# Optimization experiments

Hardware: AMD Instinct MI355X
Metric: run time of the kernel (lower is better)

## Reference

```python
import jax, jax.numpy as jnp
import numpy as np

N, F, H = 4096, 512, 64
TEMP = 1.0
EPS = 1e-6


def _lin_init(k, fi, fo):
    s = 1.0 / np.sqrt(fi)
    return jax.random.uniform(k, (fi, fo), jnp.float32, -s, s)


def setup_inputs() -> dict:
    key = jax.random.key(0)
    ks = jax.random.split(key, 8)
    adj = jax.random.uniform(ks[0], (N, N), jnp.float32)
    adj = 0.5 * (adj + adj.T)  # symmetric dense adjacency
    x = jax.random.normal(ks[1], (N, F), jnp.float32)
    return {
        'adj': adj,
        'x': x,
        'Wg': _lin_init(ks[2], F, H), 'bg': jnp.zeros((H,), jnp.float32),
        'Wa1': _lin_init(ks[3], H, H), 'ba1': jnp.zeros((H,), jnp.float32),
        'Wa2': _lin_init(ks[4], H, F), 'ba2': jnp.zeros((F,), jnp.float32),
        'Wx1': _lin_init(ks[5], H, H), 'bx1': jnp.zeros((H,), jnp.float32),
        'Wx2': _lin_init(ks[6], H, F), 'bx2': jnp.zeros((F,), jnp.float32),
    }


def _relaxed_bernoulli_st(probs, noise_logistic, temp):
    # pyro RelaxedBernoulliStraightThrough.rsample(): gumbel-sigmoid + hard round w/ ST grad
    p = jnp.clip(probs, EPS, 1.0 - EPS)
    logits = jnp.log(p) - jnp.log1p(-p)
    soft = jax.nn.sigmoid((logits + noise_logistic) / temp)
    hard = jnp.round(soft)
    return soft + jax.lax.stop_gradient(hard - soft)


def _logistic_noise(k, shape):
    u = jax.random.uniform(k, shape, jnp.float32, EPS, 1.0 - EPS)
    return jnp.log(u) - jnp.log1p(-u)


def reference(adj, x, Wg, bg, Wa1, ba1, Wa2, ba2, Wx1, bx1, Wx2, bx2):
    nkey = jax.random.key(42)
    k1, k2 = jax.random.split(nkey)
    # GCN_Body, 1 layer (dropout is eval no-op): h = relu(A @ (X W) + b)
    h = jax.nn.relu(adj @ (x @ Wg) + bg)            # [N, H]
    # MLPA: Z = Linear(ReLU(Linear(h)))
    Z = jax.nn.relu(h @ Wa1 + ba1) @ Wa2 + ba2      # [N, F]
    adj_logits = Z @ Z.T                            # [N, N]
    edge_probs = jax.nn.sigmoid(adj_logits)
    a = _relaxed_bernoulli_st(edge_probs, _logistic_noise(k1, (N, N)), TEMP)
    a = jnp.triu(a, 1)
    a = a + a.T
    # normalize_adj: fill_diagonal_(1); D^{-1/2} A D^{-1/2} (diag matmuls == row/col scaling)
    i = jnp.arange(N)
    a = a.at[i, i].set(1.0)
    d = a.sum(1) ** -0.5                            # [N]
    adj_norm = d[:, None] * a * d[None, :]
    # MLPX feature mask
    mask_logits = jax.nn.relu(h @ Wx1 + bx1) @ Wx2 + bx2  # [N, F]
    mask_probs = jax.nn.sigmoid(mask_logits)
    mask = _relaxed_bernoulli_st(mask_probs, _logistic_noise(k2, (N, F)), TEMP)
    x_new = x * mask
    return (adj_norm, x_new, adj_logits)
```

## Files before the change

### kernel.cpp

```cpp
#include <hip/hip_runtime.h>
#include <cstdint>
#include <cmath>

#define NN 4096
#define FF 512
#define HH 64
#define KSPLIT 8

typedef unsigned short ushort_t;
typedef short bf16x8 __attribute__((ext_vector_type(8)));
typedef float f32x4 __attribute__((ext_vector_type(4)));

__host__ __device__ __forceinline__ uint32_t rotl32(uint32_t x, int r) {
    return (x << r) | (x >> (32 - r));
}

__host__ __device__ __forceinline__ void threefry2x32(uint32_t ks0, uint32_t ks1,
                                                      uint32_t x0, uint32_t x1,
                                                      uint32_t& o0, uint32_t& o1) {
    uint32_t ks2 = ks0 ^ ks1 ^ 0x1BD11BDAu;
    x0 += ks0; x1 += ks1;
    x0 += x1; x1 = rotl32(x1, 13); x1 ^= x0;
    x0 += x1; x1 = rotl32(x1, 15); x1 ^= x0;
    x0 += x1; x1 = rotl32(x1, 26); x1 ^= x0;
    x0 += x1; x1 = rotl32(x1,  6); x1 ^= x0;
    x0 += ks1; x1 += ks2 + 1u;
    x0 += x1; x1 = rotl32(x1, 17); x1 ^= x0;
    x0 += x1; x1 = rotl32(x1, 29); x1 ^= x0;
    x0 += x1; x1 = rotl32(x1, 16); x1 ^= x0;
    x0 += x1; x1 = rotl32(x1, 24); x1 ^= x0;
    x0 += ks2; x1 += ks0 + 2u;
    x0 += x1; x1 = rotl32(x1, 13); x1 ^= x0;
    x0 += x1; x1 = rotl32(x1, 15); x1 ^= x0;
    x0 += x1; x1 = rotl32(x1, 26); x1 ^= x0;
    x0 += x1; x1 = rotl32(x1,  6); x1 ^= x0;
    x0 += ks0; x1 += ks1 + 3u;
    x0 += x1; x1 = rotl32(x1, 17); x1 ^= x0;
    x0 += x1; x1 = rotl32(x1, 29); x1 ^= x0;
    x0 += x1; x1 = rotl32(x1, 16); x1 ^= x0;
    x0 += x1; x1 = rotl32(x1, 24); x1 ^= x0;
    x0 += ks1; x1 += ks2 + 4u;
    x0 += x1; x1 = rotl32(x1, 13); x1 ^= x0;
    x0 += x1; x1 = rotl32(x1, 15); x1 ^= x0;
    x0 += x1; x1 = rotl32(x1, 26); x1 ^= x0;
    x0 += x1; x1 = rotl32(x1,  6); x1 ^= x0;
    x0 += ks2; x1 += ks0 + 5u;
    o0 = x0; o1 = x1;
}

__device__ __forceinline__ uint32_t jax_bits32(uint32_t k0, uint32_t k1, uint32_t j) {
    uint32_t b0, b1;
    threefry2x32(k0, k1, 0u, j, b0, b1);
    return b0 ^ b1;
}

__device__ __forceinline__ float jax_uniform(uint32_t bits) {
    const float minv = 1e-6f;
    const float maxv = (float)(1.0 - 1e-6);
    const float span = maxv - minv;
    float f = __uint_as_float((bits >> 9) | 0x3f800000u) - 1.0f;
    float u = __fadd_rn(__fmul_rn(f, span), minv);
    return fmaxf(minv, u);
}

__device__ __forceinline__ float hard_sample_f(float l, float u) {
    float thr = 1.0f / (1.0f + expf(l));
    return (u > thr) ? 1.0f : 0.0f;
}

__device__ __forceinline__ ushort_t f32_to_bf16_rne(float f) {
    uint32_t x = __float_as_uint(f);
    uint32_t r = (x + 0x7fffu + ((x >> 16) & 1u)) >> 16;
    return (ushort_t)r;
}


__global__ void k_xw(const float* __restrict__ x, const float* __restrict__ Wg,
                     ushort_t* __restrict__ Tt) {
    __shared__ ushort_t Tls[4][64];
    int col = threadIdx.x, ty = threadIdx.y;
    int row = blockIdx.x * 4 + ty;
    const float* xr = x + row * FF;
    float acc = 0.0f;
    #pragma unroll 4
    for (int k = 0; k < FF; ++k)
        acc += xr[k] * Wg[k * HH + col];
    Tls[ty][col] = f32_to_bf16_rne(acc);
    __syncthreads();
    int t = ty * 64 + col;
    if (t < 64) {
        uint2 v;
        ushort_t* p = (ushort_t*)&v;
        p[0] = Tls[0][t]; p[1] = Tls[1][t]; p[2] = Tls[2][t]; p[3] = Tls[3][t];
        *(uint2*)&Tt[(size_t)t * NN + blockIdx.x * 4] = v;
    }
}

__global__ void __launch_bounds__(256)
k_adjT_mfma(const float* __restrict__ adj, const ushort_t* __restrict__ Tt,
            float* __restrict__ partial) {
    __shared__ __align__(16) ushort_t As[64][72];
    __shared__ __align__(16) ushort_t Tl[64][72];
    int t = threadIdx.x;
    int lane = t & 63, w = t >> 6;
    int lr = lane & 15, lk = lane >> 4;
    int r0 = blockIdx.x * 64;
    int kb = blockIdx.y * (NN / KSPLIT);
    f32x4 acc[4] = {};
    for (int k0 = 0; k0 < NN / KSPLIT; k0 += 64) {
        __syncthreads();
        #pragma unroll
        for (int i = 0; i < 4; ++i) {
            int idx = t + i * 256;
            int rr = idx >> 4;
            int kq = (idx & 15) * 4;
            float4 v = *(const float4*)&adj[(size_t)(r0 + rr) * NN + kb + k0 + kq];
            uint32_t lo = (uint32_t)f32_to_bf16_rne(v.x) | ((uint32_t)f32_to_bf16_rne(v.y) << 16);
            uint32_t hi = (uint32_t)f32_to_bf16_rne(v.z) | ((uint32_t)f32_to_bf16_rne(v.w) << 16);
            uint2 pk = {lo, hi};
            *(uint2*)&As[rr][kq] = pk;
        }
        #pragma unroll
        for (int i = 0; i < 2; ++i) {
            int idx = t + i * 256;
            int cc = idx >> 3;
            int kq = (idx & 7) * 8;
            *(uint4*)&Tl[cc][kq] = *(const uint4*)&Tt[(size_t)cc * NN + kb + k0 + kq];
        }
        __syncthreads();
        #pragma unroll
        for (int ks = 0; ks < 2; ++ks) {
            bf16x8 a = *(const bf16x8*)&As[w * 16 + lr][ks * 32 + lk * 8];
            #pragma unroll
            for (int c = 0; c < 4; ++c) {
                bf16x8 bb = *(const bf16x8*)&Tl[c * 16 + lr][ks * 32 + lk * 8];
                acc[c] = __builtin_amdgcn_mfma_f32_16x16x32_bf16(a, bb, acc[c], 0, 0, 0);
            }
        }
    }
    float* P = partial + (size_t)blockIdx.y * NN * HH;
    #pragma unroll
    for (int c = 0; c < 4; ++c)
        #pragma unroll
        for (int reg = 0; reg < 4; ++reg)
            P[(size_t)(r0 + w * 16 + lk * 4 + reg) * HH + c * 16 + lr] = acc[c][reg];
}

__global__ void k_hred(const float* __restrict__ partial, const float* __restrict__ bg,
                       float* __restrict__ h) {
    int idx = blockIdx.x * 256 + threadIdx.x;
    float s = 0.0f;
    #pragma unroll
    for (int p = 0; p < KSPLIT; ++p) s += partial[(size_t)p * NN * HH + idx];
    float v = s + bg[idx & (HH - 1)];
    h[idx] = v > 0.0f ? v : 0.0f;
}

__global__ void __launch_bounds__(256)
k_mlpZ(const float* __restrict__ h, const float* __restrict__ W1,
       const float* __restrict__ b1, const float* __restrict__ W2,
       const float* __restrict__ b2, ushort_t* __restrict__ Zb) {
    __shared__ float W1l[HH][HH];
    __shared__ float A1l[8][HH];
    __shared__ float hl[8][HH];
    int t = threadIdx.x;
    int r0 = blockIdx.x * 8;
    for (int n = t; n < HH * HH; n += 256) ((float*)W1l)[n] = W1[n];
    for (int n = t; n < 8 * HH; n += 256) ((float*)hl)[n] = h[r0 * HH + n];
    __syncthreads();
    {
        int col = t & 63;
        int rb = t >> 6;
        #pragma unroll
        for (int rr = 0; rr < 2; ++rr) {
            int row = rb * 2 + rr;
            float acc = b1[col];
            #pragma unroll
            for (int k = 0; k < HH; ++k) acc += hl[row][k] * W1l[k][col];
            A1l[row][col] = acc > 0.0f ? acc : 0.0f;
        }
    }
    __syncthreads();
    #pragma unroll
    for (int p = 0; p < 2; ++p) {
        int col = p * 256 + t;
        float wc[HH];
        #pragma unroll
        for (int k = 0; k < HH; ++k) wc[k] = W2[k * FF + col];
        float bb = b2[col];
        #pragma unroll
        for (int row = 0; row < 8; ++row) {
            float acc = bb;
            #pragma unroll
            for (int k = 0; k < HH; ++k) acc += A1l[row][k] * wc[k];
            Zb[(size_t)(r0 + row) * FF + col] = f32_to_bf16_rne(acc);
        }
    }
}

__global__ void __launch_bounds__(256)
k_mlpM(const float* __restrict__ h, const float* __restrict__ W1,
       const float* __restrict__ b1, const float* __restrict__ W2,
       const float* __restrict__ b2, const float* __restrict__ x,
       float* __restrict__ xnew, uint32_t k20, uint32_t k21,
       float Lmin, float Lmax) {
    __shared__ float W1l[HH][HH];
    __shared__ float A1l[8][HH];
    __shared__ float hl[8][HH];
    int t = threadIdx.x;
    int r0 = blockIdx.x * 8;
    for (int n = t; n < HH * HH; n += 256) ((float*)W1l)[n] = W1[n];
    for (int n = t; n < 8 * HH; n += 256) ((float*)hl)[n] = h[r0 * HH + n];
    __syncthreads();
    {
        int col = t & 63;
        int rb = t >> 6;
        #pragma unroll
        for (int rr = 0; rr < 2; ++rr) {
            int row = rb * 2 + rr;
            float acc = b1[col];
            #pragma unroll
            for (int k = 0; k < HH; ++k) acc += hl[row][k] * W1l[k][col];
            A1l[row][col] = acc > 0.0f ? acc : 0.0f;
        }
    }
    __syncthreads();
    #pragma unroll
    for (int p = 0; p < 2; ++p) {
        int col = p * 256 + t;
        float wc[HH];
        #pragma unroll
        for (int k = 0; k < HH; ++k) wc[k] = W2[k * FF + col];
        float bb = b2[col];
        #pragma unroll
        for (int row = 0; row < 8; ++row) {
            float acc = bb;
            #pragma unroll
            for (int k = 0; k < HH; ++k) acc += A1l[row][k] * wc[k];
            float ml = acc;
            float l = ml < Lmin ? Lmin : (ml > Lmax ? Lmax : ml);
            uint32_t idx = (uint32_t)(r0 + row) * FF + (uint32_t)col;
            float u = jax_uniform(jax_bits32(k20, k21, idx));
            float m = hard_sample_f(l, u);
            size_t gi = (size_t)(r0 + row) * FF + col;
            xnew[gi] = (m != 0.0f) ? x[gi] : 0.0f;
        }
    }
}

__global__ void __launch_bounds__(256)
k_zzt_fused(const ushort_t* __restrict__ Zb, float* __restrict__ out2,
            uint32_t* __restrict__ mask, float* __restrict__ rowsum,
            uint32_t k10, uint32_t k11, float Lmin, float Lmax) {
    __shared__ __align__(16) union {
        struct { ushort_t At[128][72]; ushort_t Bt[128][72]; } s;
        float Tls[32][132];
    } sm;
    __shared__ uint32_t Wl[128][5];
    __shared__ int rs_i[128], cs_i[128];
    int t = threadIdx.x;
    int lane = t & 63, w = t >> 6;
    int lr = lane & 15, lk = lane >> 4;
    if (t < 128) { rs_i[t] = 0; cs_i[t] = 0; }
    int b = blockIdx.x, bi = 0;
    while (b >= 32 - bi) { b -= 32 - bi; ++bi; }
    int bj = bi + b;
    int rbase = bi * 128, cbase = bj * 128;
    f32x4 acc[2][8] = {};
    for (int k0 = 0; k0 < FF; k0 += 64) {
        __syncthreads();
        for (int n = t; n < 1024; n += 256) {
            int rr = n >> 3, ck = n & 7;
            *(uint4*)&sm.s.At[rr][ck * 8] = *(const uint4*)&Zb[(size_t)(rbase + rr) * FF + k0 + ck * 8];
            *(uint4*)&sm.s.Bt[rr][ck * 8] = *(const uint4*)&Zb[(size_t)(cbase + rr) * FF + k0 + ck * 8];
        }
        __syncthreads();
        #pragma unroll
        for (int ks = 0; ks < 2; ++ks) {
            bf16x8 a0 = *(const bf16x8*)&sm.s.At[w * 32 + lr][ks * 32 + lk * 8];
            bf16x8 a1 = *(const bf16x8*)&sm.s.At[w * 32 + 16 + lr][ks * 32 + lk * 8];
            #pragma unroll
            for (int j = 0; j < 8; ++j) {
                bf16x8 bb = *(const bf16x8*)&sm.s.Bt[j * 16 + lr][ks * 32 + lk * 8];
                acc[0][j] = __builtin_amdgcn_mfma_f32_16x16x32_bf16(a0, bb, acc[0][j], 0, 0, 0);
                acc[1][j] = __builtin_amdgcn_mfma_f32_16x16x32_bf16(a1, bb, acc[1][j], 0, 0, 0);
            }
        }
    }
    #pragma unroll
    for (int it = 0; it < 2; ++it) {
        int rg = rbase + w * 32 + it * 16 + lk * 4;
        #pragma unroll
        for (int reg = 0; reg < 4; ++reg)
            #pragma unroll
            for (int j = 0; j < 8; ++j)
                out2[(size_t)(rg + reg) * NN + cbase + j * 16 + lr] = acc[it][j][reg];
    }
    #pragma unroll
    for (int g = 0; g < 4; ++g) {
        __syncthreads();
        #pragma unroll
        for (int it = 0; it < 2; ++it)
            #pragma unroll
            for (int jp = 0; jp < 2; ++jp)
                #pragma unroll
                for (int reg = 0; reg < 4; ++reg)
                    sm.Tls[jp * 16 + lr][w * 32 + it * 16 + lk * 4 + reg] =
                        acc[it][g * 2 + jp][reg];
        __syncthreads();
        if (bi != bj) {
            #pragma unroll
            for (int r4 = 0; r4 < 4; ++r4) {
                int tr = r4 * 8 + (t >> 5);
                int tc = (t & 31) * 4;
                float4 v = *(const float4*)&sm.Tls[tr][tc];
                *(float4*)&out2[(size_t)(cbase + g * 32 + tr) * NN + rbase + tc] = v;
            }
        }
        {
            int rr = t >> 1, half = t & 1;
            int r = rbase + rr;
            uint32_t hw = 0;
            #pragma unroll
            for (int e = 0; e < 16; ++e) {
                int cl = half * 16 + e;
                float z = sm.Tls[cl][rr];
                int c = cbase + g * 32 + cl;
                float l = z < Lmin ? Lmin : (z > Lmax ? Lmax : z);
                int lo = r < c ? r : c;
                int hi = r < c ? c : r;
                uint32_t idx = (uint32_t)lo * NN + (uint32_t)hi;
                float u = jax_uniform(jax_bits32(k10, k11, idx));
                float thr = 1.0f / (1.0f + expf(l));
                uint32_t bit = (r == c) ? 1u : (u > thr ? 1u : 0u);
                hw |= bit << e;
            }
            uint32_t p = (uint32_t)__shfl_xor((int)hw, 1);
            if (half == 0) {
                uint32_t word = hw | (p << 16);
                Wl[rr][g] = word;
                mask[(size_t)r * (NN / 32) + (cbase >> 5) + g] = word;
                atomicAdd(&rs_i[rr], (int)__popc(word));
            }
        }
    }
    __syncthreads();
    if (bi != bj) {
        int cc = t >> 1;
        #pragma unroll
        for (int wi = 0; wi < 2; ++wi) {
            int wr = (t & 1) * 2 + wi;
            uint32_t tw = 0;
            #pragma unroll
            for (int bb = 0; bb < 32; ++bb)
                tw |= ((Wl[wr * 32 + bb][cc >> 5] >> (cc & 31)) & 1u) << bb;
            mask[(size_t)(cbase + cc) * (NN / 32) + (rbase >> 5) + wr] = tw;
            atomicAdd(&cs_i[cc], (int)__popc(tw));
        }
    }
    __syncthreads();
    if (t < 128) {
        atomicAdd(&rowsum[rbase + t], (float)rs_i[t]);
        if (bi != bj) atomicAdd(&rowsum[cbase + t], (float)cs_i[t]);
    }
}

__global__ void k_scale3(const uint32_t* __restrict__ mask,
                         const float* __restrict__ rowsum, float* __restrict__ out0) {
    size_t idx = ((size_t)blockIdx.x * 256 + threadIdx.x) * 4;
    int r = (int)(idx >> 12);
    int c = (int)(idx & 4095);
    uint32_t wv = mask[idx >> 5];
    int sh = (int)(idx & 31);
    float dr = 1.0f / sqrtf(rowsum[r]);
    float4 rc = *(const float4*)&rowsum[c];
    float4 o;
    o.x = ((wv >> (sh + 0)) & 1u) ? dr * (1.0f / sqrtf(rc.x)) : 0.0f;
    o.y = ((wv >> (sh + 1)) & 1u) ? dr * (1.0f / sqrtf(rc.y)) : 0.0f;
    o.z = ((wv >> (sh + 2)) & 1u) ? dr * (1.0f / sqrtf(rc.z)) : 0.0f;
    o.w = ((wv >> (sh + 3)) & 1u) ? dr * (1.0f / sqrtf(rc.w)) : 0.0f;
    *(float4*)&out0[idx] = o;
}

extern "C" void kernel_launch(void* const* d_in, const int* in_sizes, int n_in,
                              void* d_out, int out_size, void* d_ws, size_t ws_size,
                              hipStream_t stream) {
    const float* adj = (const float*)d_in[0];
    const float* x   = (const float*)d_in[1];
    const float* Wg  = (const float*)d_in[2];
    const float* bg  = (const float*)d_in[3];
    const float* Wa1 = (const float*)d_in[4];
    const float* ba1 = (const float*)d_in[5];
    const float* Wa2 = (const float*)d_in[6];
    const float* ba2 = (const float*)d_in[7];
    const float* Wx1 = (const float*)d_in[8];
    const float* bx1 = (const float*)d_in[9];
    const float* Wx2 = (const float*)d_in[10];
    const float* bx2 = (const float*)d_in[11];

    float* out0 = (float*)d_out;
    float* out1 = out0 + (size_t)NN * NN;
    float* out2 = out1 + (size_t)NN * FF;

    ushort_t* Tt   = (ushort_t*)d_ws;
    float* h       = (float*)((char*)d_ws + (1 << 20));
    ushort_t* Zb   = (ushort_t*)(h + NN * HH);
    float* partial = (float*)((char*)Zb + (size_t)NN * FF * 2);
    float* rowsum  = partial + (size_t)KSPLIT * NN * HH;
    uint32_t* mask = (uint32_t*)partial;

    uint32_t k1a, k1b, k2a, k2b;
    threefry2x32(0u, 42u, 0u, 0u, k1a, k1b);
    threefry2x32(0u, 42u, 0u, 1u, k2a, k2b);

    const float Lmax = (float)(std::log(1.0 - 1e-6) - std::log1p(-(1.0 - 1e-6)));
    const float Lmin = (float)(std::log(1e-6) - std::log1p(-1e-6));

    k_xw<<<NN / 4, dim3(64, 4), 0, stream>>>(x, Wg, Tt);
    k_adjT_mfma<<<dim3(64, KSPLIT), 256, 0, stream>>>(adj, Tt, partial);
    k_hred<<<NN * HH / 256, 256, 0, stream>>>(partial, bg, h);
    k_mlpZ<<<NN / 8, 256, 0, stream>>>(h, Wa1, ba1, Wa2, ba2, Zb);

    hipMemsetAsync(rowsum, 0, NN * sizeof(float), stream);
    k_zzt_fused<<<528, 256, 0, stream>>>(Zb, out2, mask, rowsum,
                                         k1a, k1b, Lmin, Lmax);
    k_scale3<<<NN * NN / 4 / 256, 256, 0, stream>>>(mask, rowsum, out0);

    k_mlpM<<<NN / 8, 256, 0, stream>>>(h, Wx1, bx1, Wx2, bx2, x, out1,
                                       k2a, k2b, Lmin, Lmax);
}
```

Before: 383.3 us.

## Fuse h reduction and both MLPs into one kernel; prefetch ZZT tiles in registers

Merges the split-K reduction of h, the MLPA (Z) head and the MLPX mask head into a single kernel, so h is no longer written to and re-read from global memory and two launches are removed. The mask MLP now runs before the ZZT kernel rather than after it. Separately, the ZZT GEMM loads the next K-slice of Z into registers while the current slice is being computed, which hides global load latency at the cost of 8 extra uint4 registers per thread. The fused MLP kernel now does more serial work per block and has an extra sync.

Result: slower. 541.6 us (+41.3%).

```diff
diff --git a/kernel.cpp b/kernel.cpp
--- a/kernel.cpp
+++ b/kernel.cpp
@@ -146,27 +146,29 @@
             P[(size_t)(r0 + w * 16 + lk * 4 + reg) * HH + c * 16 + lr] = acc[c][reg];
 }
 
-__global__ void k_hred(const float* __restrict__ partial, const float* __restrict__ bg,
-                       float* __restrict__ h) {
-    int idx = blockIdx.x * 256 + threadIdx.x;
-    float s = 0.0f;
-    #pragma unroll
-    for (int p = 0; p < KSPLIT; ++p) s += partial[(size_t)p * NN * HH + idx];
-    float v = s + bg[idx & (HH - 1)];
-    h[idx] = v > 0.0f ? v : 0.0f;
-}
-
 __global__ void __launch_bounds__(256)
-k_mlpZ(const float* __restrict__ h, const float* __restrict__ W1,
-       const float* __restrict__ b1, const float* __restrict__ W2,
-       const float* __restrict__ b2, ushort_t* __restrict__ Zb) {
+k_mlp(const float* __restrict__ partial, const float* __restrict__ bg,
+      const float* __restrict__ Wa1, const float* __restrict__ ba1,
+      const float* __restrict__ Wa2, const float* __restrict__ ba2,
+      const float* __restrict__ Wx1, const float* __restrict__ bx1,
+      const float* __restrict__ Wx2, const float* __restrict__ bx2,
+      const float* __restrict__ x, ushort_t* __restrict__ Zb,
+      float* __restrict__ xnew, uint32_t k20, uint32_t k21,
+      float Lmin, float Lmax) {
     __shared__ float W1l[HH][HH];
     __shared__ float A1l[8][HH];
     __shared__ float hl[8][HH];
     int t = threadIdx.x;
     int r0 = blockIdx.x * 8;
-    for (int n = t; n < HH * HH; n += 256) ((float*)W1l)[n] = W1[n];
-    for (int n = t; n < 8 * HH; n += 256) ((float*)hl)[n] = h[r0 * HH + n];
+    for (int n = t; n < 8 * HH; n += 256) {
+        float s = 0.0f;
+        #pragma unroll
+        for (int p = 0; p < KSPLIT; ++p)
+            s += partial[(size_t)p * NN * HH + (size_t)r0 * HH + n];
+        float v = s + bg[n & (HH - 1)];
+        ((float*)hl)[n] = v > 0.0f ? v : 0.0f;
+    }
+    for (int n = t; n < HH * HH; n += 256) ((float*)W1l)[n] = Wa1[n];
     __syncthreads();
     {
         int col = t & 63;
@@ -174,7 +176,7 @@
         #pragma unroll
         for (int rr = 0; rr < 2; ++rr) {
             int row = rb * 2 + rr;
-            float acc = b1[col];
+            float acc = ba1[col];
             #pragma unroll
             for (int k = 0; k < HH; ++k) acc += hl[row][k] * W1l[k][col];
             A1l[row][col] = acc > 0.0f ? acc : 0.0f;
@@ -186,8 +188,8 @@
         int col = p * 256 + t;
         float wc[HH];
         #pragma unroll
-        for (int k = 0; k < HH; ++k) wc[k] = W2[k * FF + col];
-        float bb = b2[col];
+        for (int k = 0; k < HH; ++k) wc[k] = Wa2[k * FF + col];
+        float bb = ba2[col];
         #pragma unroll
         for (int row = 0; row < 8; ++row) {
             float acc = bb;
@@ -196,21 +198,8 @@
             Zb[(size_t)(r0 + row) * FF + col] = f32_to_bf16_rne(acc);
         }
     }
-}
-
-__global__ void __launch_bounds__(256)
-k_mlpM(const float* __restrict__ h, const float* __restrict__ W1,
-       const float* __restrict__ b1, const float* __restrict__ W2,
-       const float* __restrict__ b2, const float* __restrict__ x,
-       float* __restrict__ xnew, uint32_t k20, uint32_t k21,
-       float Lmin, float Lmax) {
-    __shared__ float W1l[HH][HH];
-    __shared__ float A1l[8][HH];
-    __shared__ float hl[8][HH];
-    int t = threadIdx.x;
-    int r0 = blockIdx.x * 8;
-    for (int n = t; n < HH * HH; n += 256) ((float*)W1l)[n] = W1[n];
-    for (int n = t; n < 8 * HH; n += 256) ((float*)hl)[n] = h[r0 * HH + n];
+    __syncthreads();
+    for (int n = t; n < HH * HH; n += 256) ((float*)W1l)[n] = Wx1[n];
     __syncthreads();
     {
         int col = t & 63;
@@ -218,7 +207,7 @@
         #pragma unroll
         for (int rr = 0; rr < 2; ++rr) {
             int row = rb * 2 + rr;
-            float acc = b1[col];
+            float acc = bx1[col];
             #pragma unroll
             for (int k = 0; k < HH; ++k) acc += hl[row][k] * W1l[k][col];
             A1l[row][col] = acc > 0.0f ? acc : 0.0f;
@@ -230,8 +219,8 @@
         int col = p * 256 + t;
         float wc[HH];
         #pragma unroll
-        for (int k = 0; k < HH; ++k) wc[k] = W2[k * FF + col];
-        float bb = b2[col];
+        for (int k = 0; k < HH; ++k) wc[k] = Wx2[k * FF + col];
+        float bb = bx2[col];
         #pragma unroll
         for (int row = 0; row < 8; ++row) {
             float acc = bb;
@@ -267,12 +256,31 @@
     int bj = bi + b;
     int rbase = bi * 128, cbase = bj * 128;
     f32x4 acc[2][8] = {};
+    uint4 pa[4], pb[4];
+    #pragma unroll
+    for (int i = 0; i < 4; ++i) {
+        int n = t + i * 256;
+        int rr = n >> 3, ck = n & 7;
+        pa[i] = *(const uint4*)&Zb[(size_t)(rbase + rr) * FF + ck * 8];
+        pb[i] = *(const uint4*)&Zb[(size_t)(cbase + rr) * FF + ck * 8];
+    }
     for (int k0 = 0; k0 < FF; k0 += 64) {
         __syncthreads();
-        for (int n = t; n < 1024; n += 256) {
+        #pragma unroll
+        for (int i = 0; i < 4; ++i) {
+            int n = t + i * 256;
             int rr = n >> 3, ck = n & 7;
-            *(uint4*)&sm.s.At[rr][ck * 8] = *(const uint4*)&Zb[(size_t)(rbase + rr) * FF + k0 + ck * 8];
-            *(uint4*)&sm.s.Bt[rr][ck * 8] = *(const uint4*)&Zb[(size_t)(cbase + rr) * FF + k0 + ck * 8];
+            *(uint4*)&sm.s.At[rr][ck * 8] = pa[i];
+            *(uint4*)&sm.s.Bt[rr][ck * 8] = pb[i];
+        }
+        if (k0 + 64 < FF) {
+            #pragma unroll
+            for (int i = 0; i < 4; ++i) {
+                int n = t + i * 256;
+                int rr = n >> 3, ck = n & 7;
+                pa[i] = *(const uint4*)&Zb[(size_t)(rbase + rr) * FF + k0 + 64 + ck * 8];
+                pb[i] = *(const uint4*)&Zb[(size_t)(cbase + rr) * FF + k0 + 64 + ck * 8];
+            }
         }
         __syncthreads();
         #pragma unroll
@@ -418,14 +426,12 @@
 
     k_xw<<<NN / 4, dim3(64, 4), 0, stream>>>(x, Wg, Tt);
     k_adjT_mfma<<<dim3(64, KSPLIT), 256, 0, stream>>>(adj, Tt, partial);
-    k_hred<<<NN * HH / 256, 256, 0, stream>>>(partial, bg, h);
-    k_mlpZ<<<NN / 8, 256, 0, stream>>>(h, Wa1, ba1, Wa2, ba2, Zb);
+    k_mlp<<<NN / 8, 256, 0, stream>>>(partial, bg, Wa1, ba1, Wa2, ba2,
+                                      Wx1, bx1, Wx2, bx2, x, Zb, out1,
+                                      k2a, k2b, Lmin, Lmax);
 
     hipMemsetAsync(rowsum, 0, NN * sizeof(float), stream);
     k_zzt_fused<<<528, 256, 0, stream>>>(Zb, out2, mask, rowsum,
                                          k1a, k1b, Lmin, Lmax);
     k_scale3<<<NN * NN / 4 / 256, 256, 0, stream>>>(mask, rowsum, out0);
-
-    k_mlpM<<<NN / 8, 256, 0, stream>>>(h, Wx1, bx1, Wx2, bx2, x, out1,
-                                       k2a, k2b, Lmin, Lmax);
-}
+}
```
